# Optimization experiments

Measured on AMD Instinct MI355X. Metric: run time of the kernel, lower is better.

The kernel has to match this reference:

```python
import jax, jax.numpy as jnp
import numpy as np

H = 768
NH = 12
HD = H // NH  # 64


def setup_inputs() -> dict:
    key = jax.random.key(0)
    ks = jax.random.split(key, 12)
    B, SQ, SK = 8, 1024, 1024
    s = 1.0 / np.sqrt(H)
    return {
        "hidden_states": jax.random.normal(ks[0], (B, SQ, H), jnp.float32),
        "condition_embeddings": jax.random.normal(ks[1], (B, SK, H), jnp.float32),
        "condition_mask": jnp.ones((B, SK), jnp.float32),
        "Wq": jax.random.normal(ks[2], (H, H), jnp.float32) * s,
        "bq": jnp.zeros((H,), jnp.float32),
        "Wk": jax.random.normal(ks[3], (H, H), jnp.float32) * s,
        "bk": jnp.zeros((H,), jnp.float32),
        "Wv": jax.random.normal(ks[4], (H, H), jnp.float32) * s,
        "bv": jnp.zeros((H,), jnp.float32),
        "Wo": jax.random.normal(ks[5], (H, H), jnp.float32) * s,
        "bo": jnp.zeros((H,), jnp.float32),
        "ln_g": jnp.ones((H,), jnp.float32),
        "ln_b": jnp.zeros((H,), jnp.float32),
    }


def _heads(x):
    # [B, S, H] -> [B, NH, S, HD]
    B, S, _ = x.shape
    return x.reshape(B, S, NH, HD).transpose(0, 2, 1, 3)


def reference(hidden_states, condition_embeddings, condition_mask,
              Wq, bq, Wk, bk, Wv, bv, Wo, bo, ln_g, ln_b):
    q = _heads(hidden_states @ Wq.T + bq)            # [B,NH,SQ,HD]
    k = _heads(condition_embeddings @ Wk.T + bk)     # [B,NH,SK,HD]
    v = _heads(condition_embeddings @ Wv.T + bv)     # [B,NH,SK,HD]

    scores = jnp.einsum("bhqd,bhkd->bhqk", q, k) / np.sqrt(HD)
    ext_mask = (1.0 - condition_mask)[:, None, None, :] * -10000.0
    scores = scores + ext_mask
    probs = jax.nn.softmax(scores, axis=-1)          # dropout = identity (eval)

    ctx = jnp.einsum("bhqk,bhkd->bhqd", probs, v)    # [B,NH,SQ,HD]
    B, _, SQ, _ = ctx.shape
    ctx = ctx.transpose(0, 2, 1, 3).reshape(B, SQ, H)

    out = ctx @ Wo.T + bo
    x = hidden_states + out
    mu = jnp.mean(x, axis=-1, keepdims=True)
    var = jnp.var(x, axis=-1, keepdims=True)
    return (x - mu) / jnp.sqrt(var + 1e-5) * ln_g + ln_b
```

## Files before the change

### kernel.cpp

```cpp
#include <hip/hip_runtime.h>
#include <stdint.h>

#define B_ 8
#define S_ 1024
#define H_ 768
#define NH_ 12
#define HD_ 64
#define M_ (B_*S_)

typedef __attribute__((ext_vector_type(8))) short short8;
typedef __attribute__((ext_vector_type(4))) float floatx4;

#define MFMA16(a,b,c) __builtin_amdgcn_mfma_f32_16x16x32_bf16((a),(b),(c),0,0,0)

__device__ __forceinline__ ushort f2bf(float x){
    union { float f; unsigned u; } v; v.f = x;
    unsigned r = (v.u + 0x7fffu + ((v.u >> 16) & 1u)) >> 16;
    return (ushort)r;
}

__device__ __forceinline__ void async16(const ushort* g, ushort* l){
    __builtin_amdgcn_global_load_lds(
        (const __attribute__((address_space(1))) unsigned int*)g,
        (__attribute__((address_space(3))) unsigned int*)l, 16, 0, 0);
}

__global__ __launch_bounds__(256, 8) void cvt_all(
    const float* __restrict__ hs, const float* __restrict__ ce,
    const float* __restrict__ wq, const float* __restrict__ wk,
    const float* __restrict__ wv, const float* __restrict__ wo,
    ushort* __restrict__ hsb, ushort* __restrict__ ceb,
    ushort* __restrict__ wqb, ushort* __restrict__ wkb,
    ushort* __restrict__ wvb, ushort* __restrict__ wob)
{
    const int NA = M_*H_/4;
    const int NW = H_*H_/4;
    int i = blockIdx.x*256 + threadIdx.x;
    if (i >= 2*NA + 4*NW) return;
    const float* s; ushort* d; int off;
    if (i < NA)            { s = hs; d = hsb; off = i; }
    else if (i < 2*NA)     { s = ce; d = ceb; off = i - NA; }
    else {
        int j = i - 2*NA;
        int wsel = j / NW;
        off = j - wsel*NW;
        s = (wsel==0) ? wq : (wsel==1) ? wk : (wsel==2) ? wv : wo;
        d = (wsel==0) ? wqb : (wsel==1) ? wkb : (wsel==2) ? wvb : wob;
    }
    float4 f = ((const float4*)s)[off];
    ushort4 u;
    u.x = f2bf(f.x); u.y = f2bf(f.y); u.z = f2bf(f.z); u.w = f2bf(f.w);
    ((ushort4*)d)[off] = u;
}

__device__ __forceinline__ void gemm_body(
    const ushort* __restrict__ A, const ushort* __restrict__ Bw,
    const float* __restrict__ bias, ushort* __restrict__ obf,
    float* __restrict__ of32, int mode, int bx, int by)
{
    __shared__ ushort smem[16384];
    ushort* lA = smem;
    ushort* lB = smem + 8192;
    const int K = H_;
    int tid  = threadIdx.x;
    int lane = tid & 63, wave = tid >> 6;
    int m0 = bx * 128, n0 = by * 128;
    int wm = (wave >> 1) * 64, wn = (wave & 1) * 64;
    int fr = lane & 15, quad = lane >> 4, quad4 = quad*4;

    floatx4 acc[4][4];
    #pragma unroll
    for (int mt=0;mt<4;mt++)
        #pragma unroll
        for (int nt=0;nt<4;nt++)
            acc[mt][nt] = (floatx4){0.f,0.f,0.f,0.f};

    int row0 = tid >> 3;
    int csw  = ((tid & 7) ^ (row0 & 7)) * 8;
    const ushort* Ap[4]; const ushort* Bp[4];
    ushort* ldA_[4]; ushort* ldB_[4];
    #pragma unroll
    for (int j=0;j<4;j++){
        int row = row0 + 32*j;
        Ap[j] = A  + (size_t)(m0 + row) * K + csw;
        Bp[j] = Bw + (size_t)(n0 + row) * K + csw;
        ldA_[j] = lA + (tid + 256*j)*8;
        ldB_[j] = lB + (tid + 256*j)*8;
    }

    for (int k0 = 0; k0 < K; k0 += 64){
        #pragma unroll
        for (int j=0;j<4;j++) async16(Ap[j] + k0, ldA_[j]);
        #pragma unroll
        for (int j=0;j<4;j++) async16(Bp[j] + k0, ldB_[j]);
        __syncthreads();
        #pragma unroll
        for (int kk=0; kk<2; kk++){
            short8 af[4], bfr[4];
            #pragma unroll
            for (int t=0;t<4;t++){
                int ra = wm + t*16 + fr;
                int rb = wn + t*16 + fr;
                af[t]  = *(const short8*)&lA[ra*64 + (((kk*4+quad) ^ (ra&7))<<3)];
                bfr[t] = *(const short8*)&lB[rb*64 + (((kk*4+quad) ^ (rb&7))<<3)];
            }
            #pragma unroll
            for (int mt=0;mt<4;mt++)
                #pragma unroll
                for (int nt=0;nt<4;nt++)
                    acc[mt][nt] = MFMA16(af[mt], bfr[nt], acc[mt][nt]);
        }
        __syncthreads();
    }

    float bv_[4];
    #pragma unroll
    for (int nt=0;nt<4;nt++) bv_[nt] = bias[n0 + wn + nt*16 + fr];

    if (mode == 0){
        #pragma unroll
        for (int mt=0;mt<4;mt++){
            int rb = m0 + wm + mt*16 + quad4;
            #pragma unroll
            for (int nt=0;nt<4;nt++){
                int col = n0 + wn + nt*16 + fr;
                #pragma unroll
                for (int r=0;r<4;r++)
                    obf[(size_t)(rb + r)*H_ + col] = f2bf(acc[mt][nt][r] + bv_[nt]);
            }
        }
    } else if (mode == 1){
        int bb = m0 >> 10, q0 = m0 & 1023;
        #pragma unroll
        for (int nh=0; nh<2; nh++){
            __syncthreads();
            if ((wave & 1) == nh){
                #pragma unroll
                for (int mt=0;mt<4;mt++){
                    int ql = wm + mt*16 + quad4;
                    #pragma unroll
                    for (int nt=0;nt<4;nt++){
                        int dl = nt*16 + fr;
                        ushort4 u;
                        u.x = f2bf(acc[mt][nt][0] + bv_[nt]);
                        u.y = f2bf(acc[mt][nt][1] + bv_[nt]);
                        u.z = f2bf(acc[mt][nt][2] + bv_[nt]);
                        u.w = f2bf(acc[mt][nt][3] + bv_[nt]);
                        *(ushort4*)&smem[dl*136 + ql] = u;
                    }
                }
            }
            __syncthreads();
            int head = by*2 + nh;
            #pragma unroll
            for (int jj=0;jj<4;jj++){
                int mI = tid + 256*jj;
                int d  = mI >> 4;
                int qc = (mI & 15) * 8;
                short8 v = *(const short8*)&smem[d*136 + qc];
                *(short8*)&obf[((size_t)((bb*NH_ + head)*HD_ + d))*S_ + q0 + qc] = v;
            }
        }
    } else {
        #pragma unroll
        for (int mt=0;mt<4;mt++){
            int rb = m0 + wm + mt*16 + quad4;
            #pragma unroll
            for (int nt=0;nt<4;nt++){
                int col = n0 + wn + nt*16 + fr;
                #pragma unroll
                for (int r=0;r<4;r++)
                    of32[(size_t)(rb + r)*H_ + col] = acc[mt][nt][r] + bv_[nt];
            }
        }
    }
}

__global__ __launch_bounds__(256, 3) void gemm_qkv(
    const ushort* __restrict__ hsb, const ushort* __restrict__ ceb,
    const ushort* __restrict__ wqb, const ushort* __restrict__ wkb,
    const ushort* __restrict__ wvb,
    const float* __restrict__ bq, const float* __restrict__ bk,
    const float* __restrict__ bv,
    ushort* __restrict__ Qb, ushort* __restrict__ Kb, ushort* __restrict__ Vtb)
{
    int z = blockIdx.z;
    const ushort* A  = (z==0) ? hsb : ceb;
    const ushort* Bw = (z==0) ? wqb : (z==1) ? wkb : wvb;
    const float* bias = (z==0) ? bq : (z==1) ? bk : bv;
    ushort* obf = (z==0) ? Qb : (z==1) ? Kb : Vtb;
    gemm_body(A, Bw, bias, obf, nullptr, (z==2) ? 1 : 0, blockIdx.x, blockIdx.y);
}

__global__ __launch_bounds__(256, 3) void gemm_o(
    const ushort* __restrict__ ctxb, const ushort* __restrict__ wob,
    const float* __restrict__ bo, float* __restrict__ proj)
{
    gemm_body(ctxb, wob, bo, nullptr, proj, 2, blockIdx.x, blockIdx.y);
}

__global__ __launch_bounds__(256, 3) void attn(
    const ushort* __restrict__ Q, const ushort* __restrict__ Kc,
    const ushort* __restrict__ Vt, const float* __restrict__ mask,
    ushort* __restrict__ ctx)
{
    __shared__ ushort lK[64*64];
    __shared__ ushort lV[64*64];
    __shared__ ushort lP[4][32*72];
    __shared__ float  lmask[S_];
    __shared__ float  linv[4][32];

    const float SC = 0.125f * 1.44269504f;

    int bid = blockIdx.x;
    int qt = bid & 7;
    int h  = (bid >> 3) % NH_;
    int b  = bid / (8*NH_);

    int tid  = threadIdx.x;
    int lane = tid & 63, w = tid >> 6;
    int fr = lane & 15, quad = lane >> 4;
    int quad4 = quad*4, sw = fr & 7;

    for (int i = tid; i < S_; i += 256)
        lmask[i] = (1.0f - mask[b*S_ + i]) * -14426.95f;

    short8 qf[2][2];
    #pragma unroll
    for (int nq=0;nq<2;nq++){
        const ushort* Qp = Q + (size_t)(b*S_ + qt*128 + w*32 + nq*16 + fr)*H_ + h*HD_ + quad*8;
        qf[nq][0] = *(const short8*)(Qp);
        qf[nq][1] = *(const short8*)(Qp + 32);
    }

    floatx4 O[2][4];
    #pragma unroll
    for (int mt=0;mt<2;mt++)
        #pragma unroll
        for (int nt=0;nt<4;nt++)
            O[mt][nt] = (floatx4){0.f,0.f,0.f,0.f};
    float rs0 = 0.f, rs1 = 0.f;

    int n0 = tid,       r0 = n0 >> 3, c0 = (n0 & 7) ^ (r0 & 7);
    int n1 = 256 + tid, r1 = n1 >> 3, c1 = (n1 & 7) ^ (r1 & 7);
    const ushort* pK0 = Kc + (size_t)(b*S_ + r0)*H_ + h*HD_ + c0*8;
    const ushort* pK1 = Kc + (size_t)(b*S_ + r1)*H_ + h*HD_ + c1*8;
    const ushort* pV0 = Vt + ((size_t)(b*NH_ + h)*HD_ + r0)*S_ + c0*8;
    const ushort* pV1 = Vt + ((size_t)(b*NH_ + h)*HD_ + r1)*S_ + c1*8;
    ushort* dK0 = &lK[n0*8]; ushort* dK1 = &lK[n1*8];
    ushort* dV0 = &lV[n0*8]; ushort* dV1 = &lV[n1*8];

    ushort* lPw = &lP[w][0];

    for (int kt = 0; kt < 16; kt++){
        __syncthreads();
        async16(pK0, dK0); async16(pK1, dK1);
        async16(pV0, dV0); async16(pV1, dV1);
        pK0 += (size_t)64*H_; pK1 += (size_t)64*H_;
        pV0 += 64; pV1 += 64;
        __syncthreads();

        float4 mk4[4];
        #pragma unroll
        for (int mk=0;mk<4;mk++)
            mk4[mk] = *(const float4*)&lmask[kt*64 + mk*16 + quad4];

        short8 kf[4][2];
        #pragma unroll
        for (int mk=0;mk<4;mk++){
            int row = mk*16 + fr;
            kf[mk][0] = *(const short8*)&lK[row*64 + ((quad     ^ sw)<<3)];
            kf[mk][1] = *(const short8*)&lK[row*64 + (((4+quad) ^ sw)<<3)];
        }
        floatx4 st[2][4];
        #pragma unroll
        for (int nq=0;nq<2;nq++)
            #pragma unroll
            for (int mk=0;mk<4;mk++){
                floatx4 a = (floatx4){0.f,0.f,0.f,0.f};
                a = MFMA16(kf[mk][0], qf[nq][0], a);
                a = MFMA16(kf[mk][1], qf[nq][1], a);
                st[nq][mk] = a;
            }

        #pragma unroll
        for (int nq=0;nq<2;nq++){
            #pragma unroll
            for (int mk=0;mk<4;mk++){
                floatx4 s = st[nq][mk];
                #pragma unroll
                for (int r=0;r<4;r++)
                    s[r] = __builtin_amdgcn_exp2f(s[r]*SC + mk4[mk][r]);
                if (nq == 0) rs0 += (s[0]+s[1]) + (s[2]+s[3]);
                else         rs1 += (s[0]+s[1]) + (s[2]+s[3]);
                unsigned lo = __builtin_amdgcn_perm(__float_as_uint(s[1]), __float_as_uint(s[0]), 0x07060302u);
                unsigned hi = __builtin_amdgcn_perm(__float_as_uint(s[3]), __float_as_uint(s[2]), 0x07060302u);
                uint2 pk; pk.x = lo; pk.y = hi;
                *(uint2*)&lPw[(nq*16 + fr)*72 + mk*16 + quad4] = pk;
            }
        }

        short8 vf[4][2];
        #pragma unroll
        for (int nt=0;nt<4;nt++){
            int row = nt*16 + fr;
            vf[nt][0] = *(const short8*)&lV[row*64 + ((quad     ^ sw)<<3)];
            vf[nt][1] = *(const short8*)&lV[row*64 + (((4+quad) ^ sw)<<3)];
        }
        short8 pf[2][2];
        #pragma unroll
        for (int mt=0;mt<2;mt++){
            pf[mt][0] = *(const short8*)&lPw[(mt*16+fr)*72 + quad*8];
            pf[mt][1] = *(const short8*)&lPw[(mt*16+fr)*72 + 32 + quad*8];
        }
        #pragma unroll
        for (int mt=0;mt<2;mt++)
            #pragma unroll
            for (int nt=0;nt<4;nt++){
                O[mt][nt] = MFMA16(pf[mt][0], vf[nt][0], O[mt][nt]);
                O[mt][nt] = MFMA16(pf[mt][1], vf[nt][1], O[mt][nt]);
            }
    }

    rs0 += __shfl_xor(rs0, 16); rs0 += __shfl_xor(rs0, 32);
    rs1 += __shfl_xor(rs1, 16); rs1 += __shfl_xor(rs1, 32);
    if (lane < 16){
        linv[w][fr]      = 1.0f / rs0;
        linv[w][16 + fr] = 1.0f / rs1;
    }
    int tokbase = b*S_ + qt*128 + w*32;
    #pragma unroll
    for (int mt=0;mt<2;mt++){
        float4 iv = *(const float4*)&linv[w][mt*16 + quad4];
        #pragma unroll
        for (int nt=0;nt<4;nt++)
            #pragma unroll
            for (int r=0;r<4;r++){
                int tok = tokbase + mt*16 + quad4 + r;
                ctx[(size_t)tok*H_ + h*HD_ + nt*16 + fr] = f2bf(O[mt][nt][r] * (&iv.x)[r]);
            }
    }
}

__global__ __launch_bounds__(256, 4) void resid_ln(
    const float* __restrict__ proj, const float* __restrict__ hs,
    const float* __restrict__ g, const float* __restrict__ be,
    float* __restrict__ out)
{
    int row = blockIdx.x;
    int tid = threadIdx.x;
    const float* p = proj + (size_t)row*H_;
    const float* x = hs   + (size_t)row*H_;
    float v[3]; float s = 0.f, s2 = 0.f;
    #pragma unroll
    for (int j=0;j<3;j++){
        float t = p[tid + j*256] + x[tid + j*256];
        v[j] = t; s += t; s2 += t*t;
    }
    #pragma unroll
    for (int off=1; off<64; off<<=1){
        s  += __shfl_xor(s,  off);
        s2 += __shfl_xor(s2, off);
    }
    __shared__ float rs[4], rs2[4];
    if ((tid & 63) == 0){ rs[tid>>6] = s; rs2[tid>>6] = s2; }
    __syncthreads();
    s  = rs[0]+rs[1]+rs[2]+rs[3];
    s2 = rs2[0]+rs2[1]+rs2[2]+rs2[3];
    float mu  = s * (1.f/H_);
    float var = s2*(1.f/H_) - mu*mu;
    float rinv = rsqrtf(var + 1e-5f);
    float* o = out + (size_t)row*H_;
    #pragma unroll
    for (int j=0;j<3;j++){
        int c = tid + j*256;
        o[c] = (v[j]-mu)*rinv*g[c] + be[c];
    }
}

extern "C" void kernel_launch(void* const* d_in, const int* in_sizes, int n_in,
                              void* d_out, int out_size, void* d_ws, size_t ws_size,
                              hipStream_t stream)
{
    (void)in_sizes; (void)n_in; (void)out_size; (void)ws_size;
    const float* hs   = (const float*)d_in[0];
    const float* ce   = (const float*)d_in[1];
    const float* mask = (const float*)d_in[2];
    const float* Wq   = (const float*)d_in[3];
    const float* bq   = (const float*)d_in[4];
    const float* Wk   = (const float*)d_in[5];
    const float* bk   = (const float*)d_in[6];
    const float* Wv   = (const float*)d_in[7];
    const float* bv   = (const float*)d_in[8];
    const float* Wo   = (const float*)d_in[9];
    const float* bo   = (const float*)d_in[10];
    const float* lg   = (const float*)d_in[11];
    const float* lb   = (const float*)d_in[12];
    float* out = (float*)d_out;

    char* ws = (char*)d_ws;
    const size_t SZ_ACT = (size_t)M_*H_*2;
    const size_t SZ_W   = (size_t)H_*H_*2;
    ushort* hsb  = (ushort*)(ws);
    ushort* ceb  = (ushort*)(ws + SZ_ACT);
    ushort* wqb  = (ushort*)(ws + 2*SZ_ACT);
    ushort* wkb  = (ushort*)(ws + 2*SZ_ACT + 1*SZ_W);
    ushort* wvb  = (ushort*)(ws + 2*SZ_ACT + 2*SZ_W);
    ushort* wob  = (ushort*)(ws + 2*SZ_ACT + 3*SZ_W);
    ushort* Qb   = (ushort*)(ws + 2*SZ_ACT + 4*SZ_W);
    ushort* Kb   = (ushort*)(ws + 3*SZ_ACT + 4*SZ_W);
    ushort* Vtb  = (ushort*)(ws + 4*SZ_ACT + 4*SZ_W);
    ushort* ctxb = (ushort*)(ws + 5*SZ_ACT + 4*SZ_W);
    float*  proj = (float*)(ws);

    int ncvt = 2*(M_*H_/4) + 4*(H_*H_/4);
    cvt_all<<<dim3((ncvt+255)/256), dim3(256), 0, stream>>>(
        hs, ce, Wq, Wk, Wv, Wo, hsb, ceb, wqb, wkb, wvb, wob);

    gemm_qkv<<<dim3(M_/128, H_/128, 3), dim3(256), 0, stream>>>(
        hsb, ceb, wqb, wkb, wvb, bq, bk, bv, Qb, Kb, Vtb);

    attn<<<dim3(B_*NH_*8), dim3(256), 0, stream>>>(Qb, Kb, Vtb, mask, ctxb);

    gemm_o<<<dim3(M_/128, H_/128), dim3(256), 0, stream>>>(ctxb, wob, bo, proj);

    resid_ln<<<dim3(M_), dim3(256), 0, stream>>>(proj, hs, lg, lb, out);
}
```

Measured before the change: 229.4 us.

## Double-buffer K/V tiles in attention and reorder block-to-tile mapping

The attention kernel now double-buffers its K and V shared-memory tiles. It prefetches the next 64-key tile with async global-to-LDS loads while computing on the current one, which cuts the two barriers per iteration to one. The block index mapping now puts the query tile outermost instead of innermost, and launch bounds drop from 3 to 2 blocks per CU to fit the doubled LDS footprint. The risks are lower occupancy and weaker L2 reuse of K/V across adjacent blocks, since the blocks that share a (batch, head) are no longer consecutive.

```diff
diff --git a/kernel.cpp b/kernel.cpp
--- a/kernel.cpp
+++ b/kernel.cpp
@@ -199,13 +199,13 @@
     gemm_body(ctxb, wob, bo, nullptr, proj, 2, blockIdx.x, blockIdx.y);
 }
 
-__global__ __launch_bounds__(256, 3) void attn(
+__global__ __launch_bounds__(256, 2) void attn(
     const ushort* __restrict__ Q, const ushort* __restrict__ Kc,
     const ushort* __restrict__ Vt, const float* __restrict__ mask,
     ushort* __restrict__ ctx)
 {
-    __shared__ ushort lK[64*64];
-    __shared__ ushort lV[64*64];
+    __shared__ ushort lK[2][64*64];
+    __shared__ ushort lV[2][64*64];
     __shared__ ushort lP[4][32*72];
     __shared__ float  lmask[S_];
     __shared__ float  linv[4][32];
@@ -213,33 +213,15 @@
     const float SC = 0.125f * 1.44269504f;
 
     int bid = blockIdx.x;
-    int qt = bid & 7;
-    int h  = (bid >> 3) % NH_;
-    int b  = bid / (8*NH_);
+    int qt = bid / 96;
+    int bh = bid - qt*96;
+    int h  = bh % NH_;
+    int b  = bh / NH_;
 
     int tid  = threadIdx.x;
     int lane = tid & 63, w = tid >> 6;
     int fr = lane & 15, quad = lane >> 4;
     int quad4 = quad*4, sw = fr & 7;
-
-    for (int i = tid; i < S_; i += 256)
-        lmask[i] = (1.0f - mask[b*S_ + i]) * -14426.95f;
-
-    short8 qf[2][2];
-    #pragma unroll
-    for (int nq=0;nq<2;nq++){
-        const ushort* Qp = Q + (size_t)(b*S_ + qt*128 + w*32 + nq*16 + fr)*H_ + h*HD_ + quad*8;
-        qf[nq][0] = *(const short8*)(Qp);
-        qf[nq][1] = *(const short8*)(Qp + 32);
-    }
-
-    floatx4 O[2][4];
-    #pragma unroll
-    for (int mt=0;mt<2;mt++)
-        #pragma unroll
-        for (int nt=0;nt<4;nt++)
-            O[mt][nt] = (floatx4){0.f,0.f,0.f,0.f};
-    float rs0 = 0.f, rs1 = 0.f;
 
     int n0 = tid,       r0 = n0 >> 3, c0 = (n0 & 7) ^ (r0 & 7);
     int n1 = 256 + tid, r1 = n1 >> 3, c1 = (n1 & 7) ^ (r1 & 7);
@@ -247,18 +229,46 @@
     const ushort* pK1 = Kc + (size_t)(b*S_ + r1)*H_ + h*HD_ + c1*8;
     const ushort* pV0 = Vt + ((size_t)(b*NH_ + h)*HD_ + r0)*S_ + c0*8;
     const ushort* pV1 = Vt + ((size_t)(b*NH_ + h)*HD_ + r1)*S_ + c1*8;
-    ushort* dK0 = &lK[n0*8]; ushort* dK1 = &lK[n1*8];
-    ushort* dV0 = &lV[n0*8]; ushort* dV1 = &lV[n1*8];
+
+    async16(pK0, &lK[0][n0*8]); async16(pK1, &lK[0][n1*8]);
+    async16(pV0, &lV[0][n0*8]); async16(pV1, &lV[0][n1*8]);
+    pK0 += (size_t)64*H_; pK1 += (size_t)64*H_;
+    pV0 += 64; pV1 += 64;
+
+    for (int i = tid; i < S_; i += 256)
+        lmask[i] = (1.0f - mask[b*S_ + i]) * -14426.95f;
+
+    short8 qf[2][2];
+    #pragma unroll
+    for (int nq=0;nq<2;nq++){
+        const ushort* Qp = Q + (size_t)(b*S_ + qt*128 + w*32 + nq*16 + fr)*H_ + h*HD_ + quad*8;
+        qf[nq][0] = *(const short8*)(Qp);
+        qf[nq][1] = *(const short8*)(Qp + 32);
+    }
+
+    floatx4 O[2][4];
+    #pragma unroll
+    for (int mt=0;mt<2;mt++)
+        #pragma unroll
+        for (int nt=0;nt<4;nt++)
+            O[mt][nt] = (floatx4){0.f,0.f,0.f,0.f};
+    float rs0 = 0.f, rs1 = 0.f;
 
     ushort* lPw = &lP[w][0];
 
+    __syncthreads();
+
+    int cur = 0;
     for (int kt = 0; kt < 16; kt++){
-        __syncthreads();
-        async16(pK0, dK0); async16(pK1, dK1);
-        async16(pV0, dV0); async16(pV1, dV1);
-        pK0 += (size_t)64*H_; pK1 += (size_t)64*H_;
-        pV0 += 64; pV1 += 64;
-        __syncthreads();
+        if (kt < 15){
+            int nxt = cur ^ 1;
+            async16(pK0, &lK[nxt][n0*8]); async16(pK1, &lK[nxt][n1*8]);
+            async16(pV0, &lV[nxt][n0*8]); async16(pV1, &lV[nxt][n1*8]);
+            pK0 += (size_t)64*H_; pK1 += (size_t)64*H_;
+            pV0 += 64; pV1 += 64;
+        }
+        const ushort* Kl = lK[cur];
+        const ushort* Vl = lV[cur];
 
         float4 mk4[4];
         #pragma unroll
@@ -269,8 +279,8 @@
         #pragma unroll
         for (int mk=0;mk<4;mk++){
             int row = mk*16 + fr;
-            kf[mk][0] = *(const short8*)&lK[row*64 + ((quad     ^ sw)<<3)];
-            kf[mk][1] = *(const short8*)&lK[row*64 + (((4+quad) ^ sw)<<3)];
+            kf[mk][0] = *(const short8*)&Kl[row*64 + ((quad     ^ sw)<<3)];
+            kf[mk][1] = *(const short8*)&Kl[row*64 + (((4+quad) ^ sw)<<3)];
         }
         floatx4 st[2][4];
         #pragma unroll
@@ -304,8 +314,8 @@
         #pragma unroll
         for (int nt=0;nt<4;nt++){
             int row = nt*16 + fr;
-            vf[nt][0] = *(const short8*)&lV[row*64 + ((quad     ^ sw)<<3)];
-            vf[nt][1] = *(const short8*)&lV[row*64 + (((4+quad) ^ sw)<<3)];
+            vf[nt][0] = *(const short8*)&Vl[row*64 + ((quad     ^ sw)<<3)];
+            vf[nt][1] = *(const short8*)&Vl[row*64 + (((4+quad) ^ sw)<<3)];
         }
         short8 pf[2][2];
         #pragma unroll
@@ -320,6 +330,9 @@
                 O[mt][nt] = MFMA16(pf[mt][0], vf[nt][0], O[mt][nt]);
                 O[mt][nt] = MFMA16(pf[mt][1], vf[nt][1], O[mt][nt]);
             }
+
+        __syncthreads();
+        cur ^= 1;
     }
 
     rs0 += __shfl_xor(rs0, 16); rs0 += __shfl_xor(rs0, 32);
```

Result: no change. 228.3 us (-0.5%).

## Double attention KV tile to 128 keys and swizzle P buffer in LDS

Applied to the files above, without the earlier changes.

The attention kernel now stages 128 keys of K and V per iteration instead of 64, halving the number of barrier pairs and outer loop trips, and processes each staged tile in two 64-key halves. The P scratch buffer drops its padding and uses an XOR swizzle instead, and the inverse row sums reuse the P buffer so the separate linv array goes away. LDS per block grows (K and V tiles double), which may reduce how many blocks fit per CU, and global loads are still not overlapped with compute.

```diff
diff --git a/kernel.cpp b/kernel.cpp
--- a/kernel.cpp
+++ b/kernel.cpp
@@ -204,11 +204,10 @@
     const ushort* __restrict__ Vt, const float* __restrict__ mask,
     ushort* __restrict__ ctx)
 {
-    __shared__ ushort lK[64*64];
-    __shared__ ushort lV[64*64];
-    __shared__ ushort lP[4][32*72];
+    __shared__ ushort lK[128*64];
+    __shared__ ushort lV[64*128];
+    __shared__ ushort lP[4][32*64];
     __shared__ float  lmask[S_];
-    __shared__ float  linv[4][32];
 
     const float SC = 0.125f * 1.44269504f;
 
@@ -241,97 +240,106 @@
             O[mt][nt] = (floatx4){0.f,0.f,0.f,0.f};
     float rs0 = 0.f, rs1 = 0.f;
 
-    int n0 = tid,       r0 = n0 >> 3, c0 = (n0 & 7) ^ (r0 & 7);
-    int n1 = 256 + tid, r1 = n1 >> 3, c1 = (n1 & 7) ^ (r1 & 7);
-    const ushort* pK0 = Kc + (size_t)(b*S_ + r0)*H_ + h*HD_ + c0*8;
-    const ushort* pK1 = Kc + (size_t)(b*S_ + r1)*H_ + h*HD_ + c1*8;
-    const ushort* pV0 = Vt + ((size_t)(b*NH_ + h)*HD_ + r0)*S_ + c0*8;
-    const ushort* pV1 = Vt + ((size_t)(b*NH_ + h)*HD_ + r1)*S_ + c1*8;
-    ushort* dK0 = &lK[n0*8]; ushort* dK1 = &lK[n1*8];
-    ushort* dV0 = &lV[n0*8]; ushort* dV1 = &lV[n1*8];
+    const ushort* pK[4]; ushort* dK[4];
+    const ushort* pV[4]; ushort* dV[4];
+    #pragma unroll
+    for (int j=0;j<4;j++){
+        int n  = tid + 256*j;
+        int rk = n >> 3, ck = (n & 7) ^ (rk & 7);
+        pK[j] = Kc + (size_t)(b*S_ + rk)*H_ + h*HD_ + ck*8;
+        dK[j] = &lK[n*8];
+        int rv = n >> 4, sv = n & 15;
+        int cv = (sv & 8) | ((sv & 7) ^ (rv & 7));
+        pV[j] = Vt + ((size_t)(b*NH_ + h)*HD_ + rv)*S_ + cv*8;
+        dV[j] = &lV[n*8];
+    }
 
     ushort* lPw = &lP[w][0];
 
-    for (int kt = 0; kt < 16; kt++){
+    for (int kt = 0; kt < 8; kt++){
         __syncthreads();
-        async16(pK0, dK0); async16(pK1, dK1);
-        async16(pV0, dV0); async16(pV1, dV1);
-        pK0 += (size_t)64*H_; pK1 += (size_t)64*H_;
-        pV0 += 64; pV1 += 64;
+        #pragma unroll
+        for (int j=0;j<4;j++){ async16(pK[j], dK[j]); pK[j] += (size_t)128*H_; }
+        #pragma unroll
+        for (int j=0;j<4;j++){ async16(pV[j], dV[j]); pV[j] += 128; }
         __syncthreads();
 
-        float4 mk4[4];
-        #pragma unroll
-        for (int mk=0;mk<4;mk++)
-            mk4[mk] = *(const float4*)&lmask[kt*64 + mk*16 + quad4];
-
-        short8 kf[4][2];
-        #pragma unroll
-        for (int mk=0;mk<4;mk++){
-            int row = mk*16 + fr;
-            kf[mk][0] = *(const short8*)&lK[row*64 + ((quad     ^ sw)<<3)];
-            kf[mk][1] = *(const short8*)&lK[row*64 + (((4+quad) ^ sw)<<3)];
+        #pragma unroll
+        for (int half = 0; half < 2; half++){
+            float4 mk4[4];
+            #pragma unroll
+            for (int mk=0;mk<4;mk++)
+                mk4[mk] = *(const float4*)&lmask[kt*128 + half*64 + mk*16 + quad4];
+
+            short8 kf[4][2];
+            #pragma unroll
+            for (int mk=0;mk<4;mk++){
+                int row = half*64 + mk*16 + fr;
+                kf[mk][0] = *(const short8*)&lK[row*64 + ((quad     ^ sw)<<3)];
+                kf[mk][1] = *(const short8*)&lK[row*64 + (((4+quad) ^ sw)<<3)];
+            }
+            floatx4 st[2][4];
+            #pragma unroll
+            for (int nq=0;nq<2;nq++)
+                #pragma unroll
+                for (int mk=0;mk<4;mk++){
+                    floatx4 a = (floatx4){0.f,0.f,0.f,0.f};
+                    a = MFMA16(kf[mk][0], qf[nq][0], a);
+                    a = MFMA16(kf[mk][1], qf[nq][1], a);
+                    st[nq][mk] = a;
+                }
+
+            #pragma unroll
+            for (int nq=0;nq<2;nq++){
+                #pragma unroll
+                for (int mk=0;mk<4;mk++){
+                    floatx4 s = st[nq][mk];
+                    #pragma unroll
+                    for (int r=0;r<4;r++)
+                        s[r] = __builtin_amdgcn_exp2f(s[r]*SC + mk4[mk][r]);
+                    if (nq == 0) rs0 += (s[0]+s[1]) + (s[2]+s[3]);
+                    else         rs1 += (s[0]+s[1]) + (s[2]+s[3]);
+                    unsigned lo = __builtin_amdgcn_perm(__float_as_uint(s[1]), __float_as_uint(s[0]), 0x07060302u);
+                    unsigned hi = __builtin_amdgcn_perm(__float_as_uint(s[3]), __float_as_uint(s[2]), 0x07060302u);
+                    uint2 pk; pk.x = lo; pk.y = hi;
+                    *(uint2*)&lPw[(nq*16 + fr)*64 + (((2*mk + (quad>>1)) ^ sw)<<3) + (quad&1)*4] = pk;
+                }
+            }
+
+            short8 vf[4][2];
+            #pragma unroll
+            for (int nt=0;nt<4;nt++){
+                int row = nt*16 + fr;
+                vf[nt][0] = *(const short8*)&lV[row*128 + (((half<<3) | (quad     ^ sw))<<3)];
+                vf[nt][1] = *(const short8*)&lV[row*128 + (((half<<3) | ((4+quad) ^ sw))<<3)];
+            }
+            short8 pf[2][2];
+            #pragma unroll
+            for (int mt=0;mt<2;mt++){
+                pf[mt][0] = *(const short8*)&lPw[(mt*16+fr)*64 + ((quad     ^ sw)<<3)];
+                pf[mt][1] = *(const short8*)&lPw[(mt*16+fr)*64 + (((4+quad) ^ sw)<<3)];
+            }
+            #pragma unroll
+            for (int mt=0;mt<2;mt++)
+                #pragma unroll
+                for (int nt=0;nt<4;nt++){
+                    O[mt][nt] = MFMA16(pf[mt][0], vf[nt][0], O[mt][nt]);
+                    O[mt][nt] = MFMA16(pf[mt][1], vf[nt][1], O[mt][nt]);
+                }
         }
-        floatx4 st[2][4];
-        #pragma unroll
-        for (int nq=0;nq<2;nq++)
-            #pragma unroll
-            for (int mk=0;mk<4;mk++){
-                floatx4 a = (floatx4){0.f,0.f,0.f,0.f};
-                a = MFMA16(kf[mk][0], qf[nq][0], a);
-                a = MFMA16(kf[mk][1], qf[nq][1], a);
-                st[nq][mk] = a;
-            }
-
-        #pragma unroll
-        for (int nq=0;nq<2;nq++){
-            #pragma unroll
-            for (int mk=0;mk<4;mk++){
-                floatx4 s = st[nq][mk];
-                #pragma unroll
-                for (int r=0;r<4;r++)
-                    s[r] = __builtin_amdgcn_exp2f(s[r]*SC + mk4[mk][r]);
-                if (nq == 0) rs0 += (s[0]+s[1]) + (s[2]+s[3]);
-                else         rs1 += (s[0]+s[1]) + (s[2]+s[3]);
-                unsigned lo = __builtin_amdgcn_perm(__float_as_uint(s[1]), __float_as_uint(s[0]), 0x07060302u);
-                unsigned hi = __builtin_amdgcn_perm(__float_as_uint(s[3]), __float_as_uint(s[2]), 0x07060302u);
-                uint2 pk; pk.x = lo; pk.y = hi;
-                *(uint2*)&lPw[(nq*16 + fr)*72 + mk*16 + quad4] = pk;
-            }
-        }
-
-        short8 vf[4][2];
-        #pragma unroll
-        for (int nt=0;nt<4;nt++){
-            int row = nt*16 + fr;
-            vf[nt][0] = *(const short8*)&lV[row*64 + ((quad     ^ sw)<<3)];
-            vf[nt][1] = *(const short8*)&lV[row*64 + (((4+quad) ^ sw)<<3)];
-        }
-        short8 pf[2][2];
-        #pragma unroll
-        for (int mt=0;mt<2;mt++){
-            pf[mt][0] = *(const short8*)&lPw[(mt*16+fr)*72 + quad*8];
-            pf[mt][1] = *(const short8*)&lPw[(mt*16+fr)*72 + 32 + quad*8];
-        }
-        #pragma unroll
-        for (int mt=0;mt<2;mt++)
-            #pragma unroll
-            for (int nt=0;nt<4;nt++){
-                O[mt][nt] = MFMA16(pf[mt][0], vf[nt][0], O[mt][nt]);
-                O[mt][nt] = MFMA16(pf[mt][1], vf[nt][1], O[mt][nt]);
-            }
     }
 
     rs0 += __shfl_xor(rs0, 16); rs0 += __shfl_xor(rs0, 32);
     rs1 += __shfl_xor(rs1, 16); rs1 += __shfl_xor(rs1, 32);
+    float* linvw = (float*)&lP[w][0];
     if (lane < 16){
-        linv[w][fr]      = 1.0f / rs0;
-        linv[w][16 + fr] = 1.0f / rs1;
+        linvw[fr]      = 1.0f / rs0;
+        linvw[16 + fr] = 1.0f / rs1;
     }
     int tokbase = b*S_ + qt*128 + w*32;
     #pragma unroll
     for (int mt=0;mt<2;mt++){
-        float4 iv = *(const float4*)&linv[w][mt*16 + quad4];
+        float4 iv = *(const float4*)&linvw[mt*16 + quad4];
         #pragma unroll
         for (int nt=0;nt<4;nt++)
             #pragma unroll
```

Measured after the change: 245.8 us. 1.07x slower.

## Fuse residual add into output GEMM, vectorize LayerNorm, prioritize attention MFMAs

Applied to the files above, without the earlier changes.

The residual add moves into the output-projection GEMM epilogue, so the LayerNorm kernel reads one fp32 tensor instead of two. LayerNorm is rewritten to use 192 threads, each loading one float4 per row. The attention kernel raises wave priority around its MFMA blocks with s_setprio so matrix work is issued ahead of other waves' exp and LDS work. The cost is extra uncoalesced residual loads in the GEMM epilogue.

```diff
diff --git a/kernel.cpp b/kernel.cpp
--- a/kernel.cpp
+++ b/kernel.cpp
@@ -56,7 +56,8 @@
 __device__ __forceinline__ void gemm_body(
     const ushort* __restrict__ A, const ushort* __restrict__ Bw,
     const float* __restrict__ bias, ushort* __restrict__ obf,
-    float* __restrict__ of32, int mode, int bx, int by)
+    float* __restrict__ of32, const float* __restrict__ resid,
+    int mode, int bx, int by)
 {
     __shared__ ushort smem[16384];
     ushort* lA = smem;
@@ -169,8 +170,10 @@
             for (int nt=0;nt<4;nt++){
                 int col = n0 + wn + nt*16 + fr;
                 #pragma unroll
-                for (int r=0;r<4;r++)
-                    of32[(size_t)(rb + r)*H_ + col] = acc[mt][nt][r] + bv_[nt];
+                for (int r=0;r<4;r++){
+                    size_t idx = (size_t)(rb + r)*H_ + col;
+                    of32[idx] = acc[mt][nt][r] + bv_[nt] + resid[idx];
+                }
             }
         }
     }
@@ -189,14 +192,16 @@
     const ushort* Bw = (z==0) ? wqb : (z==1) ? wkb : wvb;
     const float* bias = (z==0) ? bq : (z==1) ? bk : bv;
     ushort* obf = (z==0) ? Qb : (z==1) ? Kb : Vtb;
-    gemm_body(A, Bw, bias, obf, nullptr, (z==2) ? 1 : 0, blockIdx.x, blockIdx.y);
+    gemm_body(A, Bw, bias, obf, nullptr, nullptr, (z==2) ? 1 : 0,
+              blockIdx.x, blockIdx.y);
 }
 
 __global__ __launch_bounds__(256, 3) void gemm_o(
     const ushort* __restrict__ ctxb, const ushort* __restrict__ wob,
-    const float* __restrict__ bo, float* __restrict__ proj)
-{
-    gemm_body(ctxb, wob, bo, nullptr, proj, 2, blockIdx.x, blockIdx.y);
+    const float* __restrict__ bo, const float* __restrict__ hs,
+    float* __restrict__ proj)
+{
+    gemm_body(ctxb, wob, bo, nullptr, proj, hs, 2, blockIdx.x, blockIdx.y);
 }
 
 __global__ __launch_bounds__(256, 3) void attn(
@@ -272,6 +277,7 @@
             kf[mk][0] = *(const short8*)&lK[row*64 + ((quad     ^ sw)<<3)];
             kf[mk][1] = *(const short8*)&lK[row*64 + (((4+quad) ^ sw)<<3)];
         }
+        __builtin_amdgcn_s_setprio(1);
         floatx4 st[2][4];
         #pragma unroll
         for (int nq=0;nq<2;nq++)
@@ -282,6 +288,7 @@
                 a = MFMA16(kf[mk][1], qf[nq][1], a);
                 st[nq][mk] = a;
             }
+        __builtin_amdgcn_s_setprio(0);
 
         #pragma unroll
         for (int nq=0;nq<2;nq++){
@@ -313,6 +320,7 @@
             pf[mt][0] = *(const short8*)&lPw[(mt*16+fr)*72 + quad*8];
             pf[mt][1] = *(const short8*)&lPw[(mt*16+fr)*72 + 32 + quad*8];
         }
+        __builtin_amdgcn_s_setprio(1);
         #pragma unroll
         for (int mt=0;mt<2;mt++)
             #pragma unroll
@@ -320,6 +328,7 @@
                 O[mt][nt] = MFMA16(pf[mt][0], vf[nt][0], O[mt][nt]);
                 O[mt][nt] = MFMA16(pf[mt][1], vf[nt][1], O[mt][nt]);
             }
+        __builtin_amdgcn_s_setprio(0);
     }
 
     rs0 += __shfl_xor(rs0, 16); rs0 += __shfl_xor(rs0, 32);
@@ -342,40 +351,37 @@
     }
 }
 
-__global__ __launch_bounds__(256, 4) void resid_ln(
-    const float* __restrict__ proj, const float* __restrict__ hs,
+__global__ __launch_bounds__(192, 4) void resid_ln(
+    const float* __restrict__ x,
     const float* __restrict__ g, const float* __restrict__ be,
     float* __restrict__ out)
 {
     int row = blockIdx.x;
     int tid = threadIdx.x;
-    const float* p = proj + (size_t)row*H_;
-    const float* x = hs   + (size_t)row*H_;
-    float v[3]; float s = 0.f, s2 = 0.f;
-    #pragma unroll
-    for (int j=0;j<3;j++){
-        float t = p[tid + j*256] + x[tid + j*256];
-        v[j] = t; s += t; s2 += t*t;
-    }
+    float4 v = ((const float4*)(x + (size_t)row*H_))[tid];
+    float s  = (v.x + v.y) + (v.z + v.w);
+    float s2 = (v.x*v.x + v.y*v.y) + (v.z*v.z + v.w*v.w);
     #pragma unroll
     for (int off=1; off<64; off<<=1){
         s  += __shfl_xor(s,  off);
         s2 += __shfl_xor(s2, off);
     }
-    __shared__ float rs[4], rs2[4];
+    __shared__ float rs[3], rs2[3];
     if ((tid & 63) == 0){ rs[tid>>6] = s; rs2[tid>>6] = s2; }
     __syncthreads();
-    s  = rs[0]+rs[1]+rs[2]+rs[3];
-    s2 = rs2[0]+rs2[1]+rs2[2]+rs2[3];
+    s  = rs[0]+rs[1]+rs[2];
+    s2 = rs2[0]+rs2[1]+rs2[2];
     float mu  = s * (1.f/H_);
     float var = s2*(1.f/H_) - mu*mu;
     float rinv = rsqrtf(var + 1e-5f);
-    float* o = out + (size_t)row*H_;
-    #pragma unroll
-    for (int j=0;j<3;j++){
-        int c = tid + j*256;
-        o[c] = (v[j]-mu)*rinv*g[c] + be[c];
-    }
+    float4 gg = ((const float4*)g)[tid];
+    float4 bb = ((const float4*)be)[tid];
+    float4 o;
+    o.x = (v.x-mu)*rinv*gg.x + bb.x;
+    o.y = (v.y-mu)*rinv*gg.y + bb.y;
+    o.z = (v.z-mu)*rinv*gg.z + bb.z;
+    o.w = (v.w-mu)*rinv*gg.w + bb.w;
+    ((float4*)(out + (size_t)row*H_))[tid] = o;
 }
 
 extern "C" void kernel_launch(void* const* d_in, const int* in_sizes, int n_in,
@@ -422,7 +428,7 @@
 
     attn<<<dim3(B_*NH_*8), dim3(256), 0, stream>>>(Qb, Kb, Vtb, mask, ctxb);
 
-    gemm_o<<<dim3(M_/128, H_/128), dim3(256), 0, stream>>>(ctxb, wob, bo, proj);
-
-    resid_ln<<<dim3(M_), dim3(256), 0, stream>>>(proj, hs, lg, lb, out);
-}
+    gemm_o<<<dim3(M_/128, H_/128), dim3(256), 0, stream>>>(ctxb, wob, bo, hs, proj);
+
+    resid_ln<<<dim3(M_), dim3(192), 0, stream>>>(proj, lg, lb, out);
+}
```

Measured after the change: 226.7 us. About the same (-1.2%).
